# Kernel optimization log

Measured on AMD Instinct MI355X. Metric: run time of the kernel, lower is better.

## Reference

```python
import jax, jax.numpy as jnp
import numpy as np

B, T, D, H, BAND = 2, 4096, 512, 8, 16
LN_EPS = 1e-5


def setup_inputs() -> dict:
    key = jax.random.key(0)
    k0, k1, k2 = jax.random.split(key, 3)
    x = jax.random.normal(k0, (B, T, D), jnp.float32)
    # nn.MultiheadAttention params: packed in_proj [3D, D] and out_proj [D, D]
    w_in = jax.random.normal(k1, (3 * D, D), jnp.float32) * 0.02
    b_in = jnp.zeros((3 * D,), jnp.float32)
    w_out = jax.random.normal(k2, (D, D), jnp.float32) * 0.02
    b_out = jnp.zeros((D,), jnp.float32)
    ln_g = jnp.ones((D,), jnp.float32)
    ln_b = jnp.zeros((D,), jnp.float32)
    return dict(x=x, ln_g=ln_g, ln_b=ln_b, w_in=w_in, b_in=b_in,
                w_out=w_out, b_out=b_out)


def reference(x, ln_g, ln_b, w_in, b_in, w_out, b_out):
    Bq, Tq, Dq = x.shape
    dh = Dq // H
    # LayerNorm
    mu = jnp.mean(x, axis=-1, keepdims=True)
    var = jnp.mean(jnp.square(x - mu), axis=-1, keepdims=True)
    h = (x - mu) * jax.lax.rsqrt(var + LN_EPS) * ln_g + ln_b
    # packed QKV projection (torch Linear: y = h @ W^T + b)
    qkv = h @ w_in.T + b_in                      # [B, T, 3D]
    q, k, v = jnp.split(qkv, 3, axis=-1)
    to_heads = lambda a: a.reshape(Bq, Tq, H, dh).transpose(0, 2, 1, 3)  # [B,H,T,dh]
    q, k, v = to_heads(q), to_heads(k), to_heads(v)
    # band-gather: each query t attends to keys in [t-BAND, t+BAND]
    Wn = 2 * BAND + 1
    offs = jnp.arange(-BAND, BAND + 1)
    idx = jnp.arange(Tq)[:, None] + offs[None, :]          # [T, Wn]
    valid = (idx >= 0) & (idx < Tq)                        # [T, Wn]
    idx_c = jnp.clip(idx, 0, Tq - 1)
    k_win = k[:, :, idx_c]                                 # [B,H,T,Wn,dh]
    v_win = v[:, :, idx_c]                                 # [B,H,T,Wn,dh]
    scale = 1.0 / np.sqrt(dh).astype(np.float32)
    scores = jnp.einsum('bhtd,bhtwd->bhtw', q * scale, k_win)
    scores = jnp.where(valid[None, None], scores, -jnp.inf)
    p = jax.nn.softmax(scores, axis=-1)                    # [B,H,T,Wn]
    o = jnp.einsum('bhtw,bhtwd->bhtd', p, v_win)           # [B,H,T,dh]
    o = o.transpose(0, 2, 1, 3).reshape(Bq, Tq, Dq)
    y = o @ w_out.T + b_out
    return x + y
```

## Files before the change

kernel.cpp:

```cpp
#include <hip/hip_runtime.h>
#include <hip/hip_bf16.h>

#define T_ 4096
#define D_ 512
#define H_ 8
#define BAND 16
#define G1_K 512

typedef float f32x4 __attribute__((ext_vector_type(4)));
typedef __bf16 bf16x8 __attribute__((ext_vector_type(8)));
typedef unsigned short us8 __attribute__((ext_vector_type(8)));
typedef unsigned short us4 __attribute__((ext_vector_type(4)));

__device__ __forceinline__ unsigned short f2b(float f) {
  union { float f; unsigned u; } v; v.f = f;
  unsigned r = v.u + 0x7fffu + ((v.u >> 16) & 1u);
  return (unsigned short)(r >> 16);
}

__device__ __forceinline__ f32x4 mfma16(bf16x8 a, bf16x8 b, f32x4 c) {
  return __builtin_amdgcn_mfma_f32_16x16x32_bf16(a, b, c, 0, 0, 0);
}

#define GLD16(gp, lp) __builtin_amdgcn_global_load_lds( \
    (const __attribute__((address_space(1))) void*)(gp), \
    (__attribute__((address_space(3))) void*)(lp), 16, 0, 0)

__global__ __launch_bounds__(256) void prep_k(const float* __restrict__ x,
                                              const float* __restrict__ g,
                                              const float* __restrict__ bt,
                                              const float* __restrict__ win,
                                              const float* __restrict__ wout,
                                              unsigned short* __restrict__ h,
                                              unsigned short* __restrict__ winb,
                                              unsigned short* __restrict__ woutb) {
  int bx = blockIdx.x;
  if (bx >= 2048) {
    int i = (bx - 2048) * 256 + threadIdx.x;
    const int n1 = 3 * D_ * D_ / 4;
    if (i < n1) {
      float4 v = ((const float4*)win)[i];
      us4 o; o.x = f2b(v.x); o.y = f2b(v.y); o.z = f2b(v.z); o.w = f2b(v.w);
      ((us4*)winb)[i] = o;
    } else {
      int j = i - n1;
      float4 v = ((const float4*)wout)[j];
      us4 o; o.x = f2b(v.x); o.y = f2b(v.y); o.z = f2b(v.z); o.w = f2b(v.w);
      ((us4*)woutb)[j] = o;
    }
    return;
  }
  int wave = threadIdx.x >> 6, lane = threadIdx.x & 63;
  size_t row = (size_t)bx * 4 + wave;
  const float4* xr = (const float4*)(x + row * D_);
  float4 a = xr[lane * 2], b = xr[lane * 2 + 1];
  float s = a.x + a.y + a.z + a.w + b.x + b.y + b.z + b.w;
  #pragma unroll
  for (int o = 32; o; o >>= 1) s += __shfl_xor(s, o, 64);
  float mu = s * (1.0f / D_);
  float d0 = a.x - mu, d1 = a.y - mu, d2 = a.z - mu, d3 = a.w - mu;
  float d4 = b.x - mu, d5 = b.y - mu, d6 = b.z - mu, d7 = b.w - mu;
  float q = d0*d0 + d1*d1 + d2*d2 + d3*d3 + d4*d4 + d5*d5 + d6*d6 + d7*d7;
  #pragma unroll
  for (int o = 32; o; o >>= 1) q += __shfl_xor(q, o, 64);
  float rstd = rsqrtf(q * (1.0f / D_) + 1e-5f);
  const float4* gr = (const float4*)g;
  const float4* br = (const float4*)bt;
  float4 g0 = gr[lane * 2], g1 = gr[lane * 2 + 1];
  float4 b0 = br[lane * 2], b1 = br[lane * 2 + 1];
  us8 o8;
  o8[0] = f2b(d0 * rstd * g0.x + b0.x);
  o8[1] = f2b(d1 * rstd * g0.y + b0.y);
  o8[2] = f2b(d2 * rstd * g0.z + b0.z);
  o8[3] = f2b(d3 * rstd * g0.w + b0.w);
  o8[4] = f2b(d4 * rstd * g1.x + b1.x);
  o8[5] = f2b(d5 * rstd * g1.y + b1.y);
  o8[6] = f2b(d6 * rstd * g1.z + b1.z);
  o8[7] = f2b(d7 * rstd * g1.w + b1.w);
  *((us8*)(h + row * D_) + lane) = o8;
}

#define SLOT_SZ 28672

__device__ __forceinline__ void stgA(const unsigned short* __restrict__ gb,
                                     unsigned short* lds, int slot, int h, int tt,
                                     int rl0, int u0, int su) {
  #pragma unroll
  for (int j = 0; j < 2; ++j) {
    int row = h * 128 + rl0 + 64 * j;
    GLD16(gb + (size_t)row * G1_K + tt * 64 + su, lds + slot * SLOT_SZ + row * 64 + u0 * 8);
  }
}
__device__ __forceinline__ void stgB(const unsigned short* __restrict__ gb,
                                     unsigned short* lds, int slot, int tt,
                                     int rl0, int u0, int su) {
  #pragma unroll
  for (int c = 0; c < 3; ++c) {
    int row = c * 64 + rl0;
    GLD16(gb + (size_t)row * G1_K + tt * 64 + su, lds + slot * SLOT_SZ + 16384 + row * 64 + u0 * 8);
  }
}

#define VMC8 asm volatile("s_waitcnt vmcnt(8)" ::: "memory")
#define VMC3 asm volatile("s_waitcnt vmcnt(3)" ::: "memory")
#define VMC0 asm volatile("s_waitcnt vmcnt(0)" ::: "memory")

#define PHASE(SLOT, PH, STAGE_STMT, WAIT_STMT) do {                                        \
    if ((PH) == 0) {                                                                       \
      _Pragma("unroll") for (int nf = 0; nf < 3; ++nf) {                                   \
        breg[nf][0] = *(const bf16x8*)(lds + (SLOT)*SLOT_SZ + boff + nf*1024 + swz0);      \
        breg[nf][1] = *(const bf16x8*)(lds + (SLOT)*SLOT_SZ + boff + nf*1024 + swz1);      \
      }                                                                                    \
    }                                                                                      \
    bf16x8 a0k0 = *(const bf16x8*)(lds + (SLOT)*SLOT_SZ + aoff + (2*(PH))*1024 + swz0);    \
    bf16x8 a0k1 = *(const bf16x8*)(lds + (SLOT)*SLOT_SZ + aoff + (2*(PH))*1024 + swz1);    \
    bf16x8 a1k0 = *(const bf16x8*)(lds + (SLOT)*SLOT_SZ + aoff + (2*(PH)+1)*1024 + swz0);  \
    bf16x8 a1k1 = *(const bf16x8*)(lds + (SLOT)*SLOT_SZ + aoff + (2*(PH)+1)*1024 + swz1);  \
    STAGE_STMT;                                                                            \
    __builtin_amdgcn_s_barrier();                                                          \
    asm volatile("s_waitcnt lgkmcnt(0)" ::: "memory");                                     \
    __builtin_amdgcn_sched_barrier(0);                                                     \
    __builtin_amdgcn_s_setprio(1);                                                         \
    _Pragma("unroll") for (int nf = 0; nf < 3; ++nf) {                                     \
      acc[2*(PH)][nf]   = mfma16(a0k0, breg[nf][0], acc[2*(PH)][nf]);                      \
      acc[2*(PH)][nf]   = mfma16(a0k1, breg[nf][1], acc[2*(PH)][nf]);                      \
      acc[2*(PH)+1][nf] = mfma16(a1k0, breg[nf][0], acc[2*(PH)+1][nf]);                    \
      acc[2*(PH)+1][nf] = mfma16(a1k1, breg[nf][1], acc[2*(PH)+1][nf]);                    \
    }                                                                                      \
    __builtin_amdgcn_s_setprio(0);                                                         \
    __builtin_amdgcn_sched_barrier(0);                                                     \
    WAIT_STMT;                                                                             \
    __builtin_amdgcn_s_barrier();                                                          \
  } while (0)

__global__ __launch_bounds__(512, 2) void gemm_qkv8(const unsigned short* __restrict__ A,
                                                    const unsigned short* __restrict__ Bw,
                                                    const float* __restrict__ bias,
                                                    unsigned short* __restrict__ C) {
  extern __shared__ char smem[];
  unsigned short* lds = (unsigned short*)smem;
  int tid = threadIdx.x;
  int lane = tid & 63, wave = tid >> 6;
  int wm = wave >> 2, wn = wave & 3;
  int fr = lane & 15, fq = lane >> 4;
  int d = blockIdx.x;
  int l = (d & 7) * 32 + (d >> 3);
  int bm = l >> 3, bn = l & 7;

  const unsigned short* Ag = A + (size_t)bm * 256 * G1_K;
  const unsigned short* Bg = Bw + (size_t)bn * 192 * G1_K;

  int rl0 = tid >> 3, u0 = tid & 7;
  int su = (u0 ^ (rl0 & 7)) * 8;

  int aoff = wm * 8192 + fr * 64;
  int boff = 16384 + (wn * 48 + fr) * 64;
  int swz0 = (fq ^ (fr & 7)) * 8;
  int swz1 = ((4 + fq) ^ (fr & 7)) * 8;

  f32x4 acc[8][3] = {};
  bf16x8 breg[3][2];

  stgB(Bg, lds, 0, 0, rl0, u0, su);
  stgA(Ag, lds, 0, 0, 0, rl0, u0, su);
  stgA(Ag, lds, 0, 1, 0, rl0, u0, su);
  stgB(Bg, lds, 1, 1, rl0, u0, su);
  VMC3;
  __builtin_amdgcn_s_barrier();

  #pragma unroll 1
  for (int i = 0; i < 3; ++i) {
    int t = 2 * i;
    PHASE(0, 0, stgA(Ag, lds, 1, 0, t + 1, rl0, u0, su), (void)0);
    PHASE(0, 1, stgA(Ag, lds, 1, 1, t + 1, rl0, u0, su), (void)0);
    PHASE(0, 2, stgB(Bg, lds, 0, t + 2, rl0, u0, su), (void)0);
    PHASE(0, 3, (void)0, VMC3);
    PHASE(1, 0, stgA(Ag, lds, 0, 0, t + 2, rl0, u0, su), (void)0);
    PHASE(1, 1, stgA(Ag, lds, 0, 1, t + 2, rl0, u0, su), (void)0);
    PHASE(1, 2, stgB(Bg, lds, 1, t + 3, rl0, u0, su), (void)0);
    PHASE(1, 3, (void)0, VMC3);
  }
  PHASE(0, 0, stgA(Ag, lds, 1, 0, 7, rl0, u0, su), (void)0);
  PHASE(0, 1, stgA(Ag, lds, 1, 1, 7, rl0, u0, su), (void)0);
  PHASE(0, 2, (void)0, (void)0);
  PHASE(0, 3, (void)0, VMC0);
  PHASE(1, 0, (void)0, (void)0);
  PHASE(1, 1, (void)0, (void)0);
  PHASE(1, 2, (void)0, (void)0);
  PHASE(1, 3, (void)0, (void)0);

  int rl = wm * 128 + fq * 4;
  int cl = wn * 48 + fr;
  float bv[3];
  #pragma unroll
  for (int nf = 0; nf < 3; ++nf) bv[nf] = bias[bn * 192 + cl + nf * 16];
  __syncthreads();
  #pragma unroll
  for (int mf = 0; mf < 8; ++mf)
    #pragma unroll
    for (int nf = 0; nf < 3; ++nf)
      #pragma unroll
      for (int r = 0; r < 4; ++r)
        lds[(rl + mf * 16 + r) * 192 + cl + nf * 16] = f2b(acc[mf][nf][r] + bv[nf]);
  __syncthreads();
  #pragma unroll
  for (int it = 0; it < 12; ++it) {
    int idx = it * 512 + tid;
    int row = idx / 24;
    int rem = (idx % 24) * 8;
    us8 v = *(const us8*)(lds + row * 192 + rem);
    *(us8*)(C + (size_t)(bm * 256 + row) * 1536 + bn * 192 + rem) = v;
  }
}

__global__ __launch_bounds__(256) void gemm_bt2(const unsigned short* __restrict__ A,
                                                const unsigned short* __restrict__ Bw,
                                                const float* __restrict__ bias,
                                                const float* __restrict__ xres,
                                                float* __restrict__ ofp,
                                                int N, int K) {
  __shared__ unsigned short AB[4 * 128 * 64];
  unsigned short* As = AB;
  unsigned short* Bs = AB + 16384;
  int tid = threadIdx.x;
  int lane = tid & 63;
  int wave = tid >> 6;
  int wm = wave >> 1, wn = wave & 1;
  int fr = lane & 15, fq = lane >> 4;
  int dd = blockIdx.x;
  int nbn = N >> 7;
  int l = (dd & 7) * (gridDim.x >> 3) + (dd >> 3);
  int bm = l / nbn, bn = l % nbn;

  const unsigned short* Ap[4];
  const unsigned short* Bp[4];
  int loff[4];
  #pragma unroll
  for (int g = 0; g < 4; ++g) {
    int s = g * 256 + tid;
    int row = s >> 3, u = s & 7;
    int uu = u ^ (row & 7);
    Ap[g] = A + (size_t)(bm * 128 + row) * K + uu * 8;
    Bp[g] = Bw + (size_t)(bn * 128 + row) * K + uu * 8;
    loff[g] = s * 16;
  }

  f32x4 acc[4][4] = {};

  #pragma unroll
  for (int g = 0; g < 4; ++g) GLD16(Ap[g], (char*)As + loff[g]);
  #pragma unroll
  for (int g = 0; g < 4; ++g) GLD16(Bp[g], (char*)Bs + loff[g]);
  #pragma unroll
  for (int g = 0; g < 4; ++g) GLD16(Ap[g] + 64, (char*)As + 16384 + loff[g]);
  #pragma unroll
  for (int g = 0; g < 4; ++g) GLD16(Bp[g] + 64, (char*)Bs + 16384 + loff[g]);
  VMC8;
  __builtin_amdgcn_s_barrier();

  #pragma unroll 1
  for (int kt = 0; kt < 8; ++kt) {
    int sl = (kt & 1) * 8192;
    bf16x8 af[4], bfr[4];
    #pragma unroll
    for (int i2 = 0; i2 < 4; ++i2) {
      int row = wm * 64 + i2 * 16 + fr;
      af[i2] = *(const bf16x8*)(As + sl + row * 64 + ((fq ^ (fr & 7)) << 3));
    }
    #pragma unroll
    for (int j = 0; j < 4; ++j) {
      int row = wn * 64 + j * 16 + fr;
      bfr[j] = *(const bf16x8*)(Bs + sl + row * 64 + ((fq ^ (fr & 7)) << 3));
    }
    #pragma unroll
    for (int i2 = 0; i2 < 4; ++i2)
      #pragma unroll
      for (int j = 0; j < 4; ++j)
        acc[i2][j] = mfma16(af[i2], bfr[j], acc[i2][j]);
    bf16x8 af1[4], bfr1[4];
    #pragma unroll
    for (int i2 = 0; i2 < 4; ++i2) {
      int row = wm * 64 + i2 * 16 + fr;
      af1[i2] = *(const bf16x8*)(As + sl + row * 64 + (((4 + fq) ^ (fr & 7)) << 3));
    }
    #pragma unroll
    for (int j = 0; j < 4; ++j) {
      int row = wn * 64 + j * 16 + fr;
      bfr1[j] = *(const bf16x8*)(Bs + sl + row * 64 + (((4 + fq) ^ (fr & 7)) << 3));
    }
    asm volatile("s_waitcnt lgkmcnt(0)" ::: "memory");
    __builtin_amdgcn_sched_barrier(0);
    __builtin_amdgcn_s_barrier();
    if (kt < 6) {
      int ko = (kt + 2) * 64;
      #pragma unroll
      for (int g = 0; g < 4; ++g) GLD16(Ap[g] + ko, (char*)As + (sl << 1) + loff[g]);
      #pragma unroll
      for (int g = 0; g < 4; ++g) GLD16(Bp[g] + ko, (char*)Bs + (sl << 1) + loff[g]);
    }
    #pragma unroll
    for (int i2 = 0; i2 < 4; ++i2)
      #pragma unroll
      for (int j = 0; j < 4; ++j)
        acc[i2][j] = mfma16(af1[i2], bfr1[j], acc[i2][j]);
    if (kt < 6)      { VMC8; }
    else if (kt == 6){ VMC0; }
    __builtin_amdgcn_s_barrier();
  }

  float* Cf = (float*)AB;
  __syncthreads();
  #pragma unroll
  for (int j = 0; j < 4; ++j)
    #pragma unroll
    for (int i2 = 0; i2 < 4; ++i2)
      #pragma unroll
      for (int r = 0; r < 4; ++r)
        Cf[(wm * 64 + i2 * 16 + fq * 4 + r) * 128 + wn * 64 + j * 16 + fr] = acc[i2][j][r];
  __syncthreads();
  #pragma unroll
  for (int it = 0; it < 16; ++it) {
    int idx = it * 256 + tid;
    int row = idx >> 5, cu = idx & 31;
    float4 c4 = ((const float4*)Cf)[idx];
    int colb = bn * 128 + cu * 4;
    float4 b4 = *(const float4*)(bias + colb);
    size_t e = (size_t)(bm * 128 + row) * N + colb;
    float4 xv = *(const float4*)(xres + e);
    float4 o;
    o.x = xv.x + c4.x + b4.x;
    o.y = xv.y + c4.y + b4.y;
    o.z = xv.z + c4.z + b4.z;
    o.w = xv.w + c4.w + b4.w;
    *(float4*)(ofp + e) = o;
  }
}

__global__ __launch_bounds__(256, 4) void attn_k(const unsigned short* __restrict__ qkv,
                                                 unsigned short* __restrict__ obuf) {
  __shared__ unsigned short Ks[96 * 72];
  __shared__ unsigned short Vt[64 * 104];
  __shared__ unsigned short Ps[64 * 104];
  int tid = threadIdx.x;
  int lane = tid & 63, wave = tid >> 6;
  int fr = lane & 15, fq = lane >> 4;
  int t0 = blockIdx.x * 64;
  int hh = blockIdx.y;
  int bb = blockIdx.z;
  size_t rowbase = (size_t)bb * T_;

  #pragma unroll
  for (int it = 0; it < 3; ++it) {
    int c = tid + it * 256;
    int r = c >> 3;
    int u = c & 7;
    int d8 = u * 8;
    int tg = t0 - BAND + r;
    us8 kv = {0,0,0,0,0,0,0,0}, vv = {0,0,0,0,0,0,0,0};
    if (tg >= 0 && tg < T_) {
      const unsigned short* p = qkv + (rowbase + tg) * 1536 + hh * 64 + d8;
      kv = *(const us8*)(p + 512);
      vv = *(const us8*)(p + 1024);
    }
    *(us8*)(Ks + r * 72 + d8) = kv;
    #pragma unroll
    for (int j = 0; j < 8; ++j) Vt[(d8 + j) * 104 + r] = vv[j];
  }

  bf16x8 qf0, qf1;
  {
    int tq = t0 + wave * 16 + fr;
    const unsigned short* qp = qkv + (rowbase + tq) * 1536 + hh * 64 + fq * 8;
    qf0 = *(const bf16x8*)qp;
    qf1 = *(const bf16x8*)(qp + 32);
  }
  __syncthreads();

  f32x4 sa[6];
  #pragma unroll
  for (int c = 0; c < 6; ++c) sa[c] = (f32x4){0.f, 0.f, 0.f, 0.f};
  #pragma unroll
  for (int c = 0; c < 6; ++c) {
    bf16x8 k0 = *(const bf16x8*)(Ks + (c * 16 + fr) * 72 + fq * 8);
    bf16x8 k1 = *(const bf16x8*)(Ks + (c * 16 + fr) * 72 + 32 + fq * 8);
    sa[c] = mfma16(qf0, k0, sa[c]);
    sa[c] = mfma16(qf1, k1, sa[c]);
  }

  float inv[4];
  float pvv[6][4];
  #pragma unroll
  for (int r = 0; r < 4; ++r) {
    int tg = t0 + wave * 16 + fq * 4 + r;
    float m = -1e30f;
    #pragma unroll
    for (int c = 0; c < 6; ++c) {
      int cg = t0 - BAND + c * 16 + fr;
      bool ok = (cg >= tg - BAND) && (cg <= tg + BAND) && (cg >= 0) && (cg < T_);
      float v = ok ? sa[c][r] * 0.125f : -1e30f;
      pvv[c][r] = v;
      m = fmaxf(m, v);
    }
    #pragma unroll
    for (int o = 8; o; o >>= 1) m = fmaxf(m, __shfl_xor(m, o, 64));
    float s = 0.0f;
    #pragma unroll
    for (int c = 0; c < 6; ++c) {
      float e = exp2f((pvv[c][r] - m) * 1.44269504f);
      pvv[c][r] = e;
      s += e;
    }
    #pragma unroll
    for (int o = 8; o; o >>= 1) s += __shfl_xor(s, o, 64);
    inv[r] = 1.0f / s;
  }

  #pragma unroll
  for (int c = 0; c < 6; ++c)
    #pragma unroll
    for (int r = 0; r < 4; ++r)
      Ps[(wave * 16 + fq * 4 + r) * 104 + c * 16 + fr] = f2b(pvv[c][r]);

  __syncthreads();

  f32x4 oa[4];
  #pragma unroll
  for (int c2 = 0; c2 < 4; ++c2) oa[c2] = (f32x4){0.f, 0.f, 0.f, 0.f};
  #pragma unroll
  for (int kk = 0; kk < 3; ++kk) {
    bf16x8 pa = *(const bf16x8*)(Ps + (wave * 16 + fr) * 104 + kk * 32 + fq * 8);
    #pragma unroll
    for (int c2 = 0; c2 < 4; ++c2) {
      bf16x8 vb = *(const bf16x8*)(Vt + (c2 * 16 + fr) * 104 + kk * 32 + fq * 8);
      oa[c2] = mfma16(pa, vb, oa[c2]);
    }
  }

  __syncthreads();
  #pragma unroll
  for (int c2 = 0; c2 < 4; ++c2)
    #pragma unroll
    for (int r = 0; r < 4; ++r)
      Ps[(wave * 16 + fq * 4 + r) * 72 + c2 * 16 + fr] = f2b(oa[c2][r] * inv[r]);
  __syncthreads();
  #pragma unroll
  for (int it = 0; it < 2; ++it) {
    int idx = it * 256 + tid;
    int row = idx >> 3, u = idx & 7;
    us8 v = *(const us8*)(Ps + row * 72 + u * 8);
    *(us8*)(obuf + (rowbase + t0 + row) * D_ + hh * 64 + u * 8) = v;
  }
}

extern "C" void kernel_launch(void* const* d_in, const int* in_sizes, int n_in,
                              void* d_out, int out_size, void* d_ws, size_t ws_size,
                              hipStream_t stream) {
  (void)in_sizes; (void)n_in; (void)out_size; (void)ws_size;
  const float* x     = (const float*)d_in[0];
  const float* ln_g  = (const float*)d_in[1];
  const float* ln_b  = (const float*)d_in[2];
  const float* w_in  = (const float*)d_in[3];
  const float* b_in  = (const float*)d_in[4];
  const float* w_out = (const float*)d_in[5];
  const float* b_out = (const float*)d_in[6];
  float* out = (float*)d_out;

  char* ws = (char*)d_ws;
  unsigned short* hb    = (unsigned short*)(ws);
  unsigned short* winb  = (unsigned short*)(ws + 8388608);
  unsigned short* woutb = (unsigned short*)(ws + 9961472);
  unsigned short* qkvb  = (unsigned short*)(ws + 10485760);
  unsigned short* obf   = (unsigned short*)(ws + 35651584);

  (void)hipFuncSetAttribute((const void*)gemm_qkv8,
                            hipFuncAttributeMaxDynamicSharedMemorySize, 114688);

  prep_k<<<3072, 256, 0, stream>>>(x, ln_g, ln_b, w_in, w_out, hb, winb, woutb);
  gemm_qkv8<<<256, 512, 114688, stream>>>(hb, winb, b_in, qkvb);
  attn_k<<<dim3(64, 8, 2), 256, 0, stream>>>(qkvb, obf);
  gemm_bt2<<<256, 256, 0, stream>>>(obf, woutb, b_out, x, out, 512, 512);
}
```

Measured before the change: 55.02 us.

## Store QKV head-major and load attention K tiles via async LDS with swizzle

The QKV GEMM epilogue now writes its output in a [section, batch, head, T, 64] layout instead of row-major [B*T, 1536], so each attention block reads contiguous per-head rows. The attention kernel loads K directly into LDS with global_load_lds using an XOR swizzle in place of padding, and clamps out-of-range rows instead of branching, relying on the existing mask. It also permutes the block index to change the order in which time tiles are scheduled. The layout change couples both kernels and makes the epilogue's global writes more scattered.

```diff
diff --git a/kernel.cpp b/kernel.cpp
--- a/kernel.cpp
+++ b/kernel.cpp
@@ -203,13 +203,18 @@
       for (int r = 0; r < 4; ++r)
         lds[(rl + mf * 16 + r) * 192 + cl + nf * 16] = f2b(acc[mf][nf][r] + bv[nf]);
   __syncthreads();
+  int bb0 = (bm * 256) >> 12;
+  int t00 = (bm * 256) & 4095;
   #pragma unroll
   for (int it = 0; it < 12; ++it) {
     int idx = it * 512 + tid;
     int row = idx / 24;
-    int rem = (idx % 24) * 8;
-    us8 v = *(const us8*)(lds + row * 192 + rem);
-    *(us8*)(C + (size_t)(bm * 256 + row) * 1536 + bn * 192 + rem) = v;
+    int u = idx % 24;
+    us8 v = *(const us8*)(lds + row * 192 + u * 8);
+    int hs = bn * 3 + (u >> 3);
+    int sec = hs >> 3, hd = hs & 7;
+    size_t dst = ((size_t)(sec * 16 + bb0 * 8 + hd) * T_ + t00 + row) * 64 + (u & 7) * 8;
+    *(us8*)(C + dst) = v;
   }
 }
 
@@ -336,41 +341,39 @@
   }
 }
 
-__global__ __launch_bounds__(256, 4) void attn_k(const unsigned short* __restrict__ qkv,
+__global__ __launch_bounds__(256, 4) void attn_k(const unsigned short* __restrict__ qkv2,
                                                  unsigned short* __restrict__ obuf) {
-  __shared__ unsigned short Ks[96 * 72];
+  __shared__ unsigned short Ks[96 * 64];
   __shared__ unsigned short Vt[64 * 104];
   __shared__ unsigned short Ps[64 * 104];
   int tid = threadIdx.x;
   int lane = tid & 63, wave = tid >> 6;
   int fr = lane & 15, fq = lane >> 4;
-  int t0 = blockIdx.x * 64;
+  int bx = blockIdx.x;
+  int t0 = ((((bx & 7) << 3) | (bx >> 3))) << 6;
   int hh = blockIdx.y;
   int bb = blockIdx.z;
-  size_t rowbase = (size_t)bb * T_;
+
+  const unsigned short* Qs = qkv2 + (size_t)(bb * 8 + hh) * T_ * 64;
+  const unsigned short* Kg = qkv2 + (size_t)(16 + bb * 8 + hh) * T_ * 64;
+  const unsigned short* Vg = qkv2 + (size_t)(32 + bb * 8 + hh) * T_ * 64;
 
   #pragma unroll
   for (int it = 0; it < 3; ++it) {
     int c = tid + it * 256;
-    int r = c >> 3;
-    int u = c & 7;
-    int d8 = u * 8;
+    int r = c >> 3, u = c & 7;
     int tg = t0 - BAND + r;
-    us8 kv = {0,0,0,0,0,0,0,0}, vv = {0,0,0,0,0,0,0,0};
-    if (tg >= 0 && tg < T_) {
-      const unsigned short* p = qkv + (rowbase + tg) * 1536 + hh * 64 + d8;
-      kv = *(const us8*)(p + 512);
-      vv = *(const us8*)(p + 1024);
-    }
-    *(us8*)(Ks + r * 72 + d8) = kv;
-    #pragma unroll
-    for (int j = 0; j < 8; ++j) Vt[(d8 + j) * 104 + r] = vv[j];
+    tg = tg < 0 ? 0 : (tg >= T_ ? T_ - 1 : tg);
+    GLD16(Kg + (size_t)tg * 64 + ((u ^ (r & 7)) << 3), Ks + c * 8);
+    us8 vv = *(const us8*)(Vg + (size_t)tg * 64 + u * 8);
+    #pragma unroll
+    for (int j = 0; j < 8; ++j) Vt[(u * 8 + j) * 104 + r] = vv[j];
   }
 
   bf16x8 qf0, qf1;
   {
     int tq = t0 + wave * 16 + fr;
-    const unsigned short* qp = qkv + (rowbase + tq) * 1536 + hh * 64 + fq * 8;
+    const unsigned short* qp = Qs + (size_t)tq * 64 + fq * 8;
     qf0 = *(const bf16x8*)qp;
     qf1 = *(const bf16x8*)(qp + 32);
   }
@@ -381,8 +384,8 @@
   for (int c = 0; c < 6; ++c) sa[c] = (f32x4){0.f, 0.f, 0.f, 0.f};
   #pragma unroll
   for (int c = 0; c < 6; ++c) {
-    bf16x8 k0 = *(const bf16x8*)(Ks + (c * 16 + fr) * 72 + fq * 8);
-    bf16x8 k1 = *(const bf16x8*)(Ks + (c * 16 + fr) * 72 + 32 + fq * 8);
+    bf16x8 k0 = *(const bf16x8*)(Ks + (c * 16 + fr) * 64 + ((fq ^ (fr & 7)) << 3));
+    bf16x8 k1 = *(const bf16x8*)(Ks + (c * 16 + fr) * 64 + (((4 + fq) ^ (fr & 7)) << 3));
     sa[c] = mfma16(qf0, k0, sa[c]);
     sa[c] = mfma16(qf1, k1, sa[c]);
   }
@@ -443,6 +446,7 @@
     for (int r = 0; r < 4; ++r)
       Ps[(wave * 16 + fq * 4 + r) * 72 + c2 * 16 + fr] = f2b(oa[c2][r] * inv[r]);
   __syncthreads();
+  size_t rowbase = (size_t)bb * T_;
   #pragma unroll
   for (int it = 0; it < 2; ++it) {
     int idx = it * 256 + tid;
```

New measurement: 54.45 us. About the same (-1.0%).
